# Kernel tuning notes

Hardware: AMD Instinct MI355X
Metric: run time of the kernel (lower is better)

## Reference

```python
import jax, jax.numpy as jnp
import numpy as np

B, D, E, H, O, TOPK = 16384, 256, 8, 128, 1, 2
THRESHOLD = 0.5
NUM_SCALES = 3
TAUS = np.linspace(5.0, 20.0, NUM_SCALES)  # MSLIFNeuron tau_range=(5,20), num_scales=3


def setup_inputs() -> dict:
    key = jax.random.key(0)
    ks = jax.random.split(key, 10)
    s = lambda fan: 1.0 / np.sqrt(fan)
    return {
        "features": jax.random.normal(ks[0], (B, D), jnp.float32),
        "Wg": jax.random.normal(ks[1], (D, E), jnp.float32) * s(D),
        "W1": jax.random.normal(ks[2], (E, D, H), jnp.float32) * s(D),
        "b1": jnp.zeros((E, H), jnp.float32),
        "Wp": jax.random.normal(ks[3], (E, H, H), jnp.float32) * s(H),
        "bp": jnp.zeros((E, H), jnp.float32),
        "mix_logit": jnp.zeros((E,), jnp.float32),
        "Wo": jax.random.normal(ks[4], (E, H, O), jnp.float32) * s(H),
        "bo": jnp.zeros((E, O), jnp.float32),
    }


def _mslif_spikes(x):
    # multi-scale LIF, single step from zero state: v_s = x * (1 - exp(-dt/tau_s))
    decays = jnp.asarray(1.0 - np.exp(-1.0 / TAUS), x.dtype)  # [S]
    v = x[:, None, :] * decays[None, :, None]                  # [B,S,D]
    return (v > THRESHOLD).astype(x.dtype).mean(axis=1)        # [B,D]


def reference(features, Wg, W1, b1, Wp, bp, mix_logit, Wo, bo):
    # gating: softmax over experts, top-k renormalized
    gate = jax.nn.softmax(features @ Wg, axis=-1)              # [B,E]
    _, idx = jax.lax.top_k(gate, TOPK)                         # [B,K]
    mask = jax.nn.one_hot(idx, E, dtype=gate.dtype).sum(1)     # [B,E]
    w = gate * mask
    w = w / (w.sum(-1, keepdims=True) + 1e-10)

    # spike generator (computed in expert forward; not used downstream)
    _spikes = _mslif_spikes(features)

    # NeuroDynArch expert: static core + plasticity mix
    core = jax.nn.relu(jnp.einsum('bd,edh->beh', features, W1) + b1[None])
    plast = jnp.tanh(jnp.einsum('beh,ehk->bek', core, Wp) + bp[None])
    mix = jax.nn.sigmoid(mix_logit)[None, :, None]             # [1,E,1]
    mixed = core * (1.0 - mix) + plast * mix                   # [B,E,H]
    out_e = jnp.einsum('beh,eho->beo', mixed, Wo) + bo[None]   # [B,E,O]
    return jnp.einsum('beo,be->bo', out_e, w)                  # [B,O]
```

## Files before the change

kernel.cpp:

```cpp
#include <hip/hip_runtime.h>

#define BB 16384
#define DD 256
#define EE 8
#define HH 128
#define RBLK 512
#define TBLK 96
#define CS_S 136

typedef __attribute__((ext_vector_type(8))) short short8;
typedef __attribute__((ext_vector_type(4))) float f32x4;

__device__ __forceinline__ ushort f2bf(float f){
    const unsigned u = __float_as_uint(f);
    return (ushort)((u + 0x7fffu + ((u >> 16) & 1u)) >> 16);
}
__device__ __forceinline__ float bf2f(ushort s){
    return __uint_as_float(((unsigned)s) << 16);
}
__device__ __forceinline__ float fast_tanh(float v){
    v = fminf(fmaxf(v, -15.0f), 15.0f);
    const float a = __expf(2.0f * v);
    return (a - 1.0f) / (a + 1.0f);
}

struct RT {
    float WgT[EE][DD];
    int   le[64];
    float lw[64];
    int   loff[64];
    int   lcount[EE];
};
union ShU { float tile[64 * 68]; RT rt; };

__device__ __forceinline__ void transpose_body(int b, int t,
    const float* __restrict__ W1, const float* __restrict__ Wp,
    ushort* __restrict__ W1t, ushort* __restrict__ Wpt, float* tile)
{
    const float* src; ushort* dst; int K;
    int k0, h0;
    if (b < 64){
        const int e = b >> 3, kt = (b >> 1) & 3, ht = b & 1;
        src = W1 + (size_t)e * DD * HH;  dst = W1t + (size_t)e * HH * DD;
        K = DD; k0 = kt * 64; h0 = ht * 64;
    } else {
        b -= 64;
        const int e = b >> 2, kt = (b >> 1) & 1, ht = b & 1;
        src = Wp + (size_t)e * HH * HH;  dst = Wpt + (size_t)e * HH * HH;
        K = HH; k0 = kt * 64; h0 = ht * 64;
    }
    #pragma unroll
    for (int j = 0; j < 4; j++){
        const int idx = t + 256 * j;
        const int kk = idx >> 4, hh = (idx & 15) * 4;
        const float4 v = *(const float4*)(src + (size_t)(k0 + kk) * HH + h0 + hh);
        *(float4*)&tile[kk * 68 + hh] = v;
    }
    __syncthreads();
    #pragma unroll
    for (int j = 0; j < 4; j++){
        const int idx = t + 256 * j;
        const int hh = idx >> 4, kk = (idx & 15) * 4;
        ushort4 o;
        o.x = f2bf(tile[(kk + 0) * 68 + hh]);
        o.y = f2bf(tile[(kk + 1) * 68 + hh]);
        o.z = f2bf(tile[(kk + 2) * 68 + hh]);
        o.w = f2bf(tile[(kk + 3) * 68 + hh]);
        *(ushort4*)&dst[(size_t)(h0 + hh) * K + k0 + kk] = o;
    }
}

__global__ __launch_bounds__(256) void prep_kernel(
    const float* __restrict__ x, const float* __restrict__ Wg,
    const float* __restrict__ W1, const float* __restrict__ Wp,
    ushort* __restrict__ W1t, ushort* __restrict__ Wpt,
    ushort* __restrict__ xbf, float* __restrict__ out,
    int* __restrict__ hist, int* __restrict__ seg_rid, float* __restrict__ seg_wgt)
{
    __shared__ ShU sh;
    const int t = threadIdx.x;
    if (blockIdx.x < TBLK){
        transpose_body(blockIdx.x, t, W1, Wp, W1t, Wpt, sh.tile);
        return;
    }
    RT* rt = &sh.rt;
    const int rb = blockIdx.x - TBLK;
    const int rowBase = rb * 32;
    if (t < 32) out[rowBase + t] = 0.0f;
    {
        const float4* g = (const float4*)(Wg + t * EE);
        const float4 a = g[0], b = g[1];
        rt->WgT[0][t] = a.x; rt->WgT[1][t] = a.y; rt->WgT[2][t] = a.z; rt->WgT[3][t] = a.w;
        rt->WgT[4][t] = b.x; rt->WgT[5][t] = b.y; rt->WgT[6][t] = b.z; rt->WgT[7][t] = b.w;
    }
    if (t < EE) rt->lcount[t] = 0;
    __syncthreads();

    const int lane = t & 63;
    const int wid  = t >> 6;

    for (int it = 0; it < 8; it++){
        const int slot = wid * 8 + it;
        const int row  = rowBase + slot;
        const float4 xv = *(const float4*)(x + row * DD + lane * 4);
        {
            ushort4 o;
            o.x = f2bf(xv.x); o.y = f2bf(xv.y); o.z = f2bf(xv.z); o.w = f2bf(xv.w);
            *(ushort4*)&xbf[(size_t)row * DD + lane * 4] = o;
        }
        float p[EE];
        #pragma unroll
        for (int e = 0; e < EE; e++){
            const float4 ww = *(const float4*)&rt->WgT[e][lane * 4];
            p[e] = xv.x * ww.x + xv.y * ww.y + xv.z * ww.z + xv.w * ww.w;
        }
        #pragma unroll
        for (int off = 32; off >= 1; off >>= 1){
            #pragma unroll
            for (int e = 0; e < EE; e++) p[e] += __shfl_down(p[e], off, 64);
        }
        if (lane == 0){
            int e0 = 0; float l0 = p[0];
            #pragma unroll
            for (int e = 1; e < EE; e++){ if (p[e] > l0){ l0 = p[e]; e0 = e; } }
            int e1 = -1; float l1 = -3.0e38f;
            #pragma unroll
            for (int e = 0; e < EE; e++){ if (e != e0 && p[e] > l1){ l1 = p[e]; e1 = e; } }
            const float tt  = __expf(l1 - l0);
            const float inv = 1.0f / (1.0f + tt);
            rt->le[slot]      = e0;  rt->lw[slot]      = inv;
            rt->le[32 + slot] = e1;  rt->lw[32 + slot] = tt * inv;
        }
    }
    __syncthreads();
    if (t < 64) rt->loff[t] = atomicAdd(&rt->lcount[rt->le[t]], 1);
    __syncthreads();
    if (t < EE) hist[t * RBLK + rb] = rt->lcount[t];
    if (t < 64){
        const int e = rt->le[t];
        const int o = (e * RBLK + rb) * 32 + rt->loff[t];
        seg_rid[o] = rowBase + (t & 31);
        seg_wgt[o] = rt->lw[t];
    }
}

__global__ __launch_bounds__(256, 3) void expert_kernel(
    const ushort* __restrict__ xbf,
    const ushort* __restrict__ W1t, const float* __restrict__ b1,
    const ushort* __restrict__ Wpt, const float* __restrict__ bp,
    const float* __restrict__ mix_logit,
    const float* __restrict__ Wo, const float* __restrict__ bo,
    const int* __restrict__ hist, const int* __restrict__ seg_rid,
    const float* __restrict__ seg_wgt, float* __restrict__ out)
{
    __shared__ ushort coreS[64 * CS_S];
    __shared__ int    Ps[RBLK + 1];
    __shared__ int    rid_s[64];
    __shared__ float  w_s[64];

    const int me = blockIdx.y;
    const int t  = threadIdx.x;

    if (t < 64){
        int h[8], incl[8];
        int s = 0;
        #pragma unroll
        for (int i = 0; i < 8; i++){ h[i] = hist[me * RBLK + t * 8 + i]; s += h[i]; incl[i] = s; }
        int run = s;
        #pragma unroll
        for (int off = 1; off < 64; off <<= 1){
            const int n = __shfl_up(run, off, 64);
            if (t >= off) run += n;
        }
        const int excl = run - s;
        #pragma unroll
        for (int i = 0; i < 8; i++) Ps[t * 8 + i] = excl + incl[i] - h[i];
        if (t == 63) Ps[RBLK] = excl + s;
    }
    __syncthreads();
    const int cnt   = Ps[RBLK];
    const int start = blockIdx.x * 64;
    if (start >= cnt) return;

    if (t < 64){
        const int s = start + t;
        if (s < cnt){
            int lo = 0, hi = RBLK - 1;
            while (lo < hi){
                const int mid = (lo + hi + 1) >> 1;
                if (Ps[mid] <= s) lo = mid; else hi = mid - 1;
            }
            const int o = (me * RBLK + lo) * 32 + (s - Ps[lo]);
            rid_s[t] = seg_rid[o];
            w_s[t]   = seg_wgt[o];
        } else { rid_s[t] = 0; w_s[t] = 0.0f; }
    }
    __syncthreads();

    const int lane = t & 63;
    const int w    = t >> 6;
    const int m16  = lane & 15;
    const int q    = lane >> 4;
    const int r0   = 32 * (w >> 1);
    const int c0   = 64 * (w & 1);

    const ushort* xrA = xbf + (size_t)rid_s[r0 + m16]      * DD;
    const ushort* xrB = xbf + (size_t)rid_s[r0 + 16 + m16] * DD;

    f32x4 acc[2][4];
    #pragma unroll
    for (int ct = 0; ct < 4; ct++){
        const float bj = b1[me * HH + c0 + ct * 16 + m16];
        #pragma unroll
        for (int rt = 0; rt < 2; rt++) acc[rt][ct] = (f32x4){bj, bj, bj, bj};
    }
    const ushort* W1te = W1t + (size_t)me * HH * DD;
    #pragma unroll
    for (int ks = 0; ks < 8; ks++){
        short8 af[2], bfr[4];
        af[0] = *(const short8*)&xrA[ks * 32 + q * 8];
        af[1] = *(const short8*)&xrB[ks * 32 + q * 8];
        #pragma unroll
        for (int ct = 0; ct < 4; ct++)
            bfr[ct] = *(const short8*)&W1te[(size_t)(c0 + ct * 16 + m16) * DD + ks * 32 + q * 8];
        #pragma unroll
        for (int rt = 0; rt < 2; rt++)
            #pragma unroll
            for (int ct = 0; ct < 4; ct++)
                acc[rt][ct] = __builtin_amdgcn_mfma_f32_16x16x32_bf16(af[rt], bfr[ct], acc[rt][ct], 0, 0, 0);
    }

    #pragma unroll
    for (int rt = 0; rt < 2; rt++)
        #pragma unroll
        for (int ct = 0; ct < 4; ct++)
            #pragma unroll
            for (int j = 0; j < 4; j++){
                const int row = r0 + rt * 16 + q * 4 + j;
                const int col = c0 + ct * 16 + m16;
                coreS[row * CS_S + col] = f2bf(fmaxf(acc[rt][ct][j], 0.0f));
            }
    __syncthreads();

    #pragma unroll
    for (int ct = 0; ct < 4; ct++){
        const float bj = bp[me * HH + c0 + ct * 16 + m16];
        #pragma unroll
        for (int rt = 0; rt < 2; rt++) acc[rt][ct] = (f32x4){bj, bj, bj, bj};
    }
    const ushort* Wpte = Wpt + (size_t)me * HH * HH;
    #pragma unroll
    for (int ks = 0; ks < 4; ks++){
        const int k0 = ks * 32;
        short8 af[2], bfr[4];
        #pragma unroll
        for (int rt = 0; rt < 2; rt++)
            af[rt] = *(const short8*)&coreS[(r0 + rt * 16 + m16) * CS_S + k0 + q * 8];
        #pragma unroll
        for (int ct = 0; ct < 4; ct++)
            bfr[ct] = *(const short8*)&Wpte[(size_t)(c0 + ct * 16 + m16) * HH + k0 + q * 8];
        #pragma unroll
        for (int rt = 0; rt < 2; rt++)
            #pragma unroll
            for (int ct = 0; ct < 4; ct++)
                acc[rt][ct] = __builtin_amdgcn_mfma_f32_16x16x32_bf16(af[rt], bfr[ct], acc[rt][ct], 0, 0, 0);
    }

    const float mv  = 1.0f / (1.0f + __expf(-mix_logit[me]));
    const float om  = 1.0f - mv;
    const float bov = bo[me];
    float wo[4];
    #pragma unroll
    for (int ct = 0; ct < 4; ct++) wo[ct] = Wo[me * HH + c0 + ct * 16 + m16];

    float red[2][4];
    #pragma unroll
    for (int rt = 0; rt < 2; rt++)
        #pragma unroll
        for (int j = 0; j < 4; j++){
            float s = 0.0f;
            const int row = r0 + rt * 16 + q * 4 + j;
            #pragma unroll
            for (int ct = 0; ct < 4; ct++){
                const int col = c0 + ct * 16 + m16;
                const float pl = fast_tanh(acc[rt][ct][j]);
                const float cv = bf2f(coreS[row * CS_S + col]);
                s = fmaf(om * cv + mv * pl, wo[ct], s);
            }
            red[rt][j] = s;
        }
    #pragma unroll
    for (int off = 8; off >= 1; off >>= 1)
        #pragma unroll
        for (int rt = 0; rt < 2; rt++)
            #pragma unroll
            for (int j = 0; j < 4; j++)
                red[rt][j] += __shfl_xor(red[rt][j], off, 64);

    if (m16 == 0){
        const float bb = (c0 == 0) ? bov : 0.0f;
        #pragma unroll
        for (int rt = 0; rt < 2; rt++)
            #pragma unroll
            for (int j = 0; j < 4; j++){
                const int row = r0 + rt * 16 + q * 4 + j;
                const float ww = w_s[row];
                if (ww != 0.0f) atomicAdd(&out[rid_s[row]], (red[rt][j] + bb) * ww);
            }
    }
}

extern "C" void kernel_launch(void* const* d_in, const int* in_sizes, int n_in,
                              void* d_out, int out_size, void* d_ws, size_t ws_size,
                              hipStream_t stream) {
    (void)in_sizes; (void)n_in; (void)out_size; (void)ws_size;
    const float* x   = (const float*)d_in[0];
    const float* Wg  = (const float*)d_in[1];
    const float* W1  = (const float*)d_in[2];
    const float* b1  = (const float*)d_in[3];
    const float* Wp  = (const float*)d_in[4];
    const float* bp  = (const float*)d_in[5];
    const float* ml  = (const float*)d_in[6];
    const float* Wo  = (const float*)d_in[7];
    const float* bo  = (const float*)d_in[8];
    float* out = (float*)d_out;

    char* ws = (char*)d_ws;
    int*    hist    = (int*)ws;
    int*    seg_rid = (int*)(ws + (16 << 10));
    float*  seg_wgt = (float*)(ws + (16 << 10) + (512 << 10));
    ushort* W1t     = (ushort*)(ws + (16 << 10) + 2 * (512 << 10));
    ushort* Wpt     = W1t + (size_t)EE * HH * DD;
    ushort* xbf     = Wpt + (size_t)EE * HH * HH;

    prep_kernel<<<TBLK + RBLK, 256, 0, stream>>>(
        x, Wg, W1, Wp, W1t, Wpt, xbf, out, hist, seg_rid, seg_wgt);
    expert_kernel<<<dim3(BB / 64, EE), 256, 0, stream>>>(
        xbf, W1t, b1, Wpt, bp, ml, Wo, bo, hist, seg_rid, seg_wgt, out);
}
```

Measured before the change: 147.0 us.

## Replace sparse routed expert dispatch with dense all-expert compute per row tile

The prep kernel now writes only a packed per-row route record (top-2 expert ids and weights). It drops the per-expert histograms, the segment scatter lists and the zeroing of the output. The expert kernel no longer does a prefix scan, binary search, gathered row loads and atomic output accumulation. Instead each 512-thread block loads a 64-row x tile into swizzled LDS via global_load_lds and evaluates all 8 experts on it, weighting unselected experts by zero. It then reduces across waves and writes the output directly, which removes routing and scatter overhead and the atomics, in exchange for about four times more MFMA work.

```diff
diff --git a/kernel.cpp b/kernel.cpp
--- a/kernel.cpp
+++ b/kernel.cpp
@@ -23,13 +23,16 @@
     const float a = __expf(2.0f * v);
     return (a - 1.0f) / (a + 1.0f);
 }
+__device__ __forceinline__ void gload_lds16(const void* g, void* l){
+    __builtin_amdgcn_global_load_lds(
+        (const __attribute__((address_space(1))) unsigned*)g,
+        (__attribute__((address_space(3))) unsigned*)l, 16, 0, 0);
+}
 
 struct RT {
     float WgT[EE][DD];
     int   le[64];
     float lw[64];
-    int   loff[64];
-    int   lcount[EE];
 };
 union ShU { float tile[64 * 68]; RT rt; };
 
@@ -74,8 +77,7 @@
     const float* __restrict__ x, const float* __restrict__ Wg,
     const float* __restrict__ W1, const float* __restrict__ Wp,
     ushort* __restrict__ W1t, ushort* __restrict__ Wpt,
-    ushort* __restrict__ xbf, float* __restrict__ out,
-    int* __restrict__ hist, int* __restrict__ seg_rid, float* __restrict__ seg_wgt)
+    ushort* __restrict__ xbf, float4* __restrict__ route)
 {
     __shared__ ShU sh;
     const int t = threadIdx.x;
@@ -86,14 +88,12 @@
     RT* rt = &sh.rt;
     const int rb = blockIdx.x - TBLK;
     const int rowBase = rb * 32;
-    if (t < 32) out[rowBase + t] = 0.0f;
     {
         const float4* g = (const float4*)(Wg + t * EE);
         const float4 a = g[0], b = g[1];
         rt->WgT[0][t] = a.x; rt->WgT[1][t] = a.y; rt->WgT[2][t] = a.z; rt->WgT[3][t] = a.w;
         rt->WgT[4][t] = b.x; rt->WgT[5][t] = b.y; rt->WgT[6][t] = b.z; rt->WgT[7][t] = b.w;
     }
-    if (t < EE) rt->lcount[t] = 0;
     __syncthreads();
 
     const int lane = t & 63;
@@ -133,180 +133,185 @@
         }
     }
     __syncthreads();
-    if (t < 64) rt->loff[t] = atomicAdd(&rt->lcount[rt->le[t]], 1);
-    __syncthreads();
-    if (t < EE) hist[t * RBLK + rb] = rt->lcount[t];
-    if (t < 64){
-        const int e = rt->le[t];
-        const int o = (e * RBLK + rb) * 32 + rt->loff[t];
-        seg_rid[o] = rowBase + (t & 31);
-        seg_wgt[o] = rt->lw[t];
-    }
-}
-
-__global__ __launch_bounds__(256, 3) void expert_kernel(
+    if (t < 32){
+        route[rowBase + t] = make_float4(__int_as_float(rt->le[t]),
+                                         __int_as_float(rt->le[32 + t]),
+                                         rt->lw[t], rt->lw[32 + t]);
+    }
+}
+
+__global__ __launch_bounds__(512, 1) void dense_kernel(
     const ushort* __restrict__ xbf,
     const ushort* __restrict__ W1t, const float* __restrict__ b1,
     const ushort* __restrict__ Wpt, const float* __restrict__ bp,
     const float* __restrict__ mix_logit,
     const float* __restrict__ Wo, const float* __restrict__ bo,
-    const int* __restrict__ hist, const int* __restrict__ seg_rid,
-    const float* __restrict__ seg_wgt, float* __restrict__ out)
+    const float4* __restrict__ route, float* __restrict__ out)
 {
-    __shared__ ushort coreS[64 * CS_S];
-    __shared__ int    Ps[RBLK + 1];
-    __shared__ int    rid_s[64];
-    __shared__ float  w_s[64];
-
-    const int me = blockIdx.y;
-    const int t  = threadIdx.x;
-
-    if (t < 64){
-        int h[8], incl[8];
-        int s = 0;
-        #pragma unroll
-        for (int i = 0; i < 8; i++){ h[i] = hist[me * RBLK + t * 8 + i]; s += h[i]; incl[i] = s; }
-        int run = s;
-        #pragma unroll
-        for (int off = 1; off < 64; off <<= 1){
-            const int n = __shfl_up(run, off, 64);
-            if (t >= off) run += n;
-        }
-        const int excl = run - s;
-        #pragma unroll
-        for (int i = 0; i < 8; i++) Ps[t * 8 + i] = excl + incl[i] - h[i];
-        if (t == 63) Ps[RBLK] = excl + s;
-    }
-    __syncthreads();
-    const int cnt   = Ps[RBLK];
-    const int start = blockIdx.x * 64;
-    if (start >= cnt) return;
-
-    if (t < 64){
-        const int s = start + t;
-        if (s < cnt){
-            int lo = 0, hi = RBLK - 1;
-            while (lo < hi){
-                const int mid = (lo + hi + 1) >> 1;
-                if (Ps[mid] <= s) lo = mid; else hi = mid - 1;
-            }
-            const int o = (me * RBLK + lo) * 32 + (s - Ps[lo]);
-            rid_s[t] = seg_rid[o];
-            w_s[t]   = seg_wgt[o];
-        } else { rid_s[t] = 0; w_s[t] = 0.0f; }
-    }
-    __syncthreads();
-
+    __shared__ ushort Xs[64 * DD];
+    __shared__ ushort coreS[4][64 * CS_S];
+    __shared__ float4 routeS[64];
+    __shared__ float  wES[4][64];
+    __shared__ float  redS[8][64];
+    __shared__ float  mvS[EE], boS[EE];
+
+    const int t = threadIdx.x;
+    const int rowBase = blockIdx.x * 64;
     const int lane = t & 63;
     const int w    = t >> 6;
+
+    if (t < 64) routeS[t] = route[rowBase + t];
+    if (t < EE){ mvS[t] = 1.0f / (1.0f + __expf(-mix_logit[t])); boS[t] = bo[t]; }
+
+    {
+        const int rsub = lane >> 5;
+        const int c    = lane & 31;
+        #pragma unroll
+        for (int i = 0; i < 4; i++){
+            const int row = w * 8 + i * 2 + rsub;
+            const int sc  = c ^ (row & 7);
+            const ushort* gp = xbf + (size_t)(rowBase + row) * DD + sc * 8;
+            gload_lds16(gp, &Xs[(w * 8 + i * 2) * DD]);
+        }
+    }
+    asm volatile("s_waitcnt vmcnt(0)" ::: "memory");
+    __syncthreads();
+
     const int m16  = lane & 15;
     const int q    = lane >> 4;
-    const int r0   = 32 * (w >> 1);
-    const int c0   = 64 * (w & 1);
-
-    const ushort* xrA = xbf + (size_t)rid_s[r0 + m16]      * DD;
-    const ushort* xrB = xbf + (size_t)rid_s[r0 + 16 + m16] * DD;
-
-    f32x4 acc[2][4];
+    const int g    = w >> 1;
+    const int half = w & 1;
+    const int c0   = 64 * half;
+    const int swz  = m16 & 7;
+    ushort* coreSg = coreS[g];
+
+    float red[4][4];
     #pragma unroll
-    for (int ct = 0; ct < 4; ct++){
-        const float bj = b1[me * HH + c0 + ct * 16 + m16];
-        #pragma unroll
-        for (int rt = 0; rt < 2; rt++) acc[rt][ct] = (f32x4){bj, bj, bj, bj};
-    }
-    const ushort* W1te = W1t + (size_t)me * HH * DD;
-    #pragma unroll
-    for (int ks = 0; ks < 8; ks++){
-        short8 af[2], bfr[4];
-        af[0] = *(const short8*)&xrA[ks * 32 + q * 8];
-        af[1] = *(const short8*)&xrB[ks * 32 + q * 8];
-        #pragma unroll
-        for (int ct = 0; ct < 4; ct++)
-            bfr[ct] = *(const short8*)&W1te[(size_t)(c0 + ct * 16 + m16) * DD + ks * 32 + q * 8];
-        #pragma unroll
-        for (int rt = 0; rt < 2; rt++)
+    for (int rt = 0; rt < 4; rt++)
+        #pragma unroll
+        for (int j = 0; j < 4; j++) red[rt][j] = 0.0f;
+
+    #pragma unroll 1
+    for (int sub = 0; sub < 2; sub++){
+        const int e = 2 * g + sub;
+
+        if ((t & 127) < 64){
+            const int row = t & 127;
+            const float4 rv = routeS[row];
+            const int e0 = __float_as_int(rv.x);
+            const int e1 = __float_as_int(rv.y);
+            wES[g][row] = (e == e0) ? rv.z : ((e == e1) ? rv.w : 0.0f);
+        }
+
+        f32x4 acc[4][4];
+        #pragma unroll
+        for (int ct = 0; ct < 4; ct++){
+            const float bj = b1[e * HH + c0 + ct * 16 + m16];
+            #pragma unroll
+            for (int rt = 0; rt < 4; rt++) acc[rt][ct] = (f32x4){bj, bj, bj, bj};
+        }
+        const ushort* W1te = W1t + (size_t)e * HH * DD;
+        #pragma unroll
+        for (int ks = 0; ks < 8; ks++){
+            const int kc = ks * 4 + q;
+            short8 af[4], bfr[4];
+            #pragma unroll
+            for (int rt = 0; rt < 4; rt++)
+                af[rt] = *(const short8*)&Xs[(rt * 16 + m16) * DD + ((kc ^ swz) * 8)];
             #pragma unroll
             for (int ct = 0; ct < 4; ct++)
-                acc[rt][ct] = __builtin_amdgcn_mfma_f32_16x16x32_bf16(af[rt], bfr[ct], acc[rt][ct], 0, 0, 0);
-    }
-
-    #pragma unroll
-    for (int rt = 0; rt < 2; rt++)
-        #pragma unroll
-        for (int ct = 0; ct < 4; ct++)
+                bfr[ct] = *(const short8*)&W1te[(size_t)(c0 + ct * 16 + m16) * DD + ks * 32 + q * 8];
+            #pragma unroll
+            for (int rt = 0; rt < 4; rt++)
+                #pragma unroll
+                for (int ct = 0; ct < 4; ct++)
+                    acc[rt][ct] = __builtin_amdgcn_mfma_f32_16x16x32_bf16(af[rt], bfr[ct], acc[rt][ct], 0, 0, 0);
+        }
+
+        #pragma unroll
+        for (int rt = 0; rt < 4; rt++)
+            #pragma unroll
+            for (int ct = 0; ct < 4; ct++)
+                #pragma unroll
+                for (int j = 0; j < 4; j++){
+                    const int row = rt * 16 + q * 4 + j;
+                    const int col = c0 + ct * 16 + m16;
+                    coreSg[row * CS_S + col] = f2bf(fmaxf(acc[rt][ct][j], 0.0f));
+                }
+        __syncthreads();
+
+        f32x4 acc2[4][4];
+        #pragma unroll
+        for (int ct = 0; ct < 4; ct++){
+            const float bj = bp[e * HH + c0 + ct * 16 + m16];
+            #pragma unroll
+            for (int rt = 0; rt < 4; rt++) acc2[rt][ct] = (f32x4){bj, bj, bj, bj};
+        }
+        const ushort* Wpte = Wpt + (size_t)e * HH * HH;
+        #pragma unroll
+        for (int ks = 0; ks < 4; ks++){
+            const int k0 = ks * 32;
+            short8 af[4], bfr[4];
+            #pragma unroll
+            for (int rt = 0; rt < 4; rt++)
+                af[rt] = *(const short8*)&coreSg[(rt * 16 + m16) * CS_S + k0 + q * 8];
+            #pragma unroll
+            for (int ct = 0; ct < 4; ct++)
+                bfr[ct] = *(const short8*)&Wpte[(size_t)(c0 + ct * 16 + m16) * HH + k0 + q * 8];
+            #pragma unroll
+            for (int rt = 0; rt < 4; rt++)
+                #pragma unroll
+                for (int ct = 0; ct < 4; ct++)
+                    acc2[rt][ct] = __builtin_amdgcn_mfma_f32_16x16x32_bf16(af[rt], bfr[ct], acc2[rt][ct], 0, 0, 0);
+        }
+
+        const float mv  = mvS[e];
+        const float om  = 1.0f - mv;
+        const float badd = (half == 0) ? boS[e] : 0.0f;
+        float wo[4];
+        #pragma unroll
+        for (int ct = 0; ct < 4; ct++) wo[ct] = Wo[e * HH + c0 + ct * 16 + m16];
+
+        #pragma unroll
+        for (int rt = 0; rt < 4; rt++)
             #pragma unroll
             for (int j = 0; j < 4; j++){
-                const int row = r0 + rt * 16 + q * 4 + j;
-                const int col = c0 + ct * 16 + m16;
-                coreS[row * CS_S + col] = f2bf(fmaxf(acc[rt][ct][j], 0.0f));
+                const int row = rt * 16 + q * 4 + j;
+                float s = 0.0f;
+                #pragma unroll
+                for (int ct = 0; ct < 4; ct++){
+                    const int col = c0 + ct * 16 + m16;
+                    const float pl = fast_tanh(acc2[rt][ct][j]);
+                    const float cv = bf2f(coreSg[row * CS_S + col]);
+                    s = fmaf(om * cv + mv * pl, wo[ct], s);
+                }
+                const float wj = wES[g][row];
+                red[rt][j] = fmaf(wj, s + badd, red[rt][j]);
             }
-    __syncthreads();
-
-    #pragma unroll
-    for (int ct = 0; ct < 4; ct++){
-        const float bj = bp[me * HH + c0 + ct * 16 + m16];
-        #pragma unroll
-        for (int rt = 0; rt < 2; rt++) acc[rt][ct] = (f32x4){bj, bj, bj, bj};
-    }
-    const ushort* Wpte = Wpt + (size_t)me * HH * HH;
-    #pragma unroll
-    for (int ks = 0; ks < 4; ks++){
-        const int k0 = ks * 32;
-        short8 af[2], bfr[4];
-        #pragma unroll
-        for (int rt = 0; rt < 2; rt++)
-            af[rt] = *(const short8*)&coreS[(r0 + rt * 16 + m16) * CS_S + k0 + q * 8];
-        #pragma unroll
-        for (int ct = 0; ct < 4; ct++)
-            bfr[ct] = *(const short8*)&Wpte[(size_t)(c0 + ct * 16 + m16) * HH + k0 + q * 8];
-        #pragma unroll
-        for (int rt = 0; rt < 2; rt++)
-            #pragma unroll
-            for (int ct = 0; ct < 4; ct++)
-                acc[rt][ct] = __builtin_amdgcn_mfma_f32_16x16x32_bf16(af[rt], bfr[ct], acc[rt][ct], 0, 0, 0);
-    }
-
-    const float mv  = 1.0f / (1.0f + __expf(-mix_logit[me]));
-    const float om  = 1.0f - mv;
-    const float bov = bo[me];
-    float wo[4];
-    #pragma unroll
-    for (int ct = 0; ct < 4; ct++) wo[ct] = Wo[me * HH + c0 + ct * 16 + m16];
-
-    float red[2][4];
-    #pragma unroll
-    for (int rt = 0; rt < 2; rt++)
-        #pragma unroll
-        for (int j = 0; j < 4; j++){
-            float s = 0.0f;
-            const int row = r0 + rt * 16 + q * 4 + j;
-            #pragma unroll
-            for (int ct = 0; ct < 4; ct++){
-                const int col = c0 + ct * 16 + m16;
-                const float pl = fast_tanh(acc[rt][ct][j]);
-                const float cv = bf2f(coreS[row * CS_S + col]);
-                s = fmaf(om * cv + mv * pl, wo[ct], s);
-            }
-            red[rt][j] = s;
-        }
+        __syncthreads();
+    }
+
     #pragma unroll
     for (int off = 8; off >= 1; off >>= 1)
         #pragma unroll
-        for (int rt = 0; rt < 2; rt++)
+        for (int rt = 0; rt < 4; rt++)
             #pragma unroll
             for (int j = 0; j < 4; j++)
                 red[rt][j] += __shfl_xor(red[rt][j], off, 64);
 
-    if (m16 == 0){
-        const float bb = (c0 == 0) ? bov : 0.0f;
-        #pragma unroll
-        for (int rt = 0; rt < 2; rt++)
-            #pragma unroll
-            for (int j = 0; j < 4; j++){
-                const int row = r0 + rt * 16 + q * 4 + j;
-                const float ww = w_s[row];
-                if (ww != 0.0f) atomicAdd(&out[rid_s[row]], (red[rt][j] + bb) * ww);
-            }
+    if (m16 == 0)
+        #pragma unroll
+        for (int rt = 0; rt < 4; rt++)
+            #pragma unroll
+            for (int j = 0; j < 4; j++)
+                redS[w][rt * 16 + q * 4 + j] = red[rt][j];
+    __syncthreads();
+
+    if (t < 64){
+        float s = 0.0f;
+        #pragma unroll
+        for (int ww = 0; ww < 8; ww++) s += redS[ww][t];
+        out[rowBase + t] = s;
     }
 }
 
@@ -325,16 +330,14 @@
     const float* bo  = (const float*)d_in[8];
     float* out = (float*)d_out;
 
-    char* ws = (char*)d_ws;
-    int*    hist    = (int*)ws;
-    int*    seg_rid = (int*)(ws + (16 << 10));
-    float*  seg_wgt = (float*)(ws + (16 << 10) + (512 << 10));
-    ushort* W1t     = (ushort*)(ws + (16 << 10) + 2 * (512 << 10));
-    ushort* Wpt     = W1t + (size_t)EE * HH * DD;
-    ushort* xbf     = Wpt + (size_t)EE * HH * HH;
+    char*   ws    = (char*)d_ws;
+    float4* route = (float4*)ws;
+    ushort* W1t   = (ushort*)(ws + (size_t)BB * 16);
+    ushort* Wpt   = W1t + (size_t)EE * HH * DD;
+    ushort* xbf   = Wpt + (size_t)EE * HH * HH;
 
     prep_kernel<<<TBLK + RBLK, 256, 0, stream>>>(
-        x, Wg, W1, Wp, W1t, Wpt, xbf, out, hist, seg_rid, seg_wgt);
-    expert_kernel<<<dim3(BB / 64, EE), 256, 0, stream>>>(
-        xbf, W1t, b1, Wpt, bp, ml, Wo, bo, hist, seg_rid, seg_wgt, out);
-}
+        x, Wg, W1, Wp, W1t, Wpt, xbf, route);
+    dense_kernel<<<BB / 64, 512, 0, stream>>>(
+        xbf, W1t, b1, Wpt, bp, ml, Wo, bo, route, out);
+}
```

Result: faster. 136.6 us (-7.1%).
